# Kernel optimization log

Measured on AMD Instinct MI355X. Metric: run time of the kernel, lower is better.

The kernel has to match this reference:

```python
import jax, jax.numpy as jnp
import numpy as np

ARITY, LABEL_DIM, H_DIM, B = 2, 128, 512, 16384
ARG_DIM = LABEL_DIM + ARITY * H_DIM


def setup_inputs() -> dict:
    key = jax.random.key(0)
    ks = jax.random.split(key, 12)
    s_lin = 1.0 / np.sqrt(ARG_DIM)
    inp = {
        "label": jax.random.normal(ks[0], (B, LABEL_DIM), jnp.float32),
        "children_h": jax.random.normal(ks[1], (ARITY, B, H_DIM), jnp.float32),
        "children_c": jax.random.normal(ks[2], (ARITY, B, H_DIM), jnp.float32),
        # torch Linear params: W (h, arg_dim), b (h,)
        "W_i": jax.random.normal(ks[3], (H_DIM, ARG_DIM), jnp.float32) * s_lin,
        "b_i": jax.random.normal(ks[4], (H_DIM,), jnp.float32) * s_lin,
        "W_o": jax.random.normal(ks[5], (H_DIM, ARG_DIM), jnp.float32) * s_lin,
        "b_o": jax.random.normal(ks[6], (H_DIM,), jnp.float32) * s_lin,
        "W_u": jax.random.normal(ks[7], (H_DIM, ARG_DIM), jnp.float32) * s_lin,
        "b_u": jax.random.normal(ks[8], (H_DIM,), jnp.float32) * s_lin,
        # forget params (xavier-ish init)
        "W_fl": jax.random.normal(ks[9], (H_DIM, LABEL_DIM), jnp.float32) * np.sqrt(2.0 / (H_DIM + LABEL_DIM)),
        "W_fs": jax.random.normal(ks[10], (ARITY, ARITY, H_DIM, H_DIM), jnp.float32) * np.sqrt(1.0 / H_DIM),
        "forget_bias": jax.random.normal(ks[11], (H_DIM,), jnp.float32) * 0.1,
    }
    return inp


def reference(label, children_h, children_c, W_i, b_i, W_o, b_o, W_u, b_u, W_fl, W_fs, forget_bias):
    arity, b, h = children_h.shape
    # x = cat([label, h_0, ..., h_{arity-1}], dim=1)  -> (B, arg_dim)
    x = jnp.concatenate([label, children_h.transpose(1, 0, 2).reshape(b, arity * h)], axis=1)
    i_gate = jax.nn.sigmoid(x @ W_i.T + b_i)
    o_gate = jax.nn.sigmoid(x @ W_o.T + b_o)
    u = jnp.tanh(x @ W_u.T + b_u)
    # per-child forget weight: [W_fl | W_fs[k,0] | ... | W_fs[k,arity-1]]  -> (arity, h, arg_dim)
    Wf = jnp.concatenate(
        [jnp.broadcast_to(W_fl, (arity,) + W_fl.shape),
         W_fs.transpose(0, 2, 1, 3).reshape(arity, h, arity * h)],
        axis=2,
    )
    # bmm (no bias inside sigmoid; forget_bias enters separately below)
    f = jax.nn.sigmoid(jnp.einsum("khd,bd->kbh", Wf, x))
    cells_composed = (f * children_c).sum(axis=0)          # (B, h)
    cells_forget_bias = forget_bias * children_c.sum(axis=0)
    next_cell = i_gate * u + cells_composed + cells_forget_bias
    out = jnp.tanh(o_gate * next_cell)
    return (next_cell, out)
```

## Files before the change

### kernel.cpp

```cpp
#include <hip/hip_runtime.h>
#include <hip/hip_bf16.h>
#include <cstdint>
#include <cstddef>

#define BROWS   16384
#define LDIM    128
#define HDIM    512
#define KDIM    1152
#define NGATES  2560

#define XB_BYTES  ((size_t)BROWS * KDIM * 2)
#define WB_BYTES  ((size_t)NGATES * KDIM * 2)

using f32x4  = __attribute__((ext_vector_type(4))) float;
using bfrag  = __attribute__((ext_vector_type(8))) short;
using short4v = __attribute__((ext_vector_type(4))) short;

__device__ __forceinline__ short f2bf(float f) {
    union { float f; uint32_t u; } a; a.f = f;
    uint32_t u = a.u;
    uint32_t lsb = (u >> 16) & 1u;
    u += 0x7fffu + lsb;
    return (short)(u >> 16);
}
__device__ __forceinline__ float bf2f(short s) {
    union { uint32_t u; float f; } a;
    a.u = ((uint32_t)(uint16_t)s) << 16;
    return a.f;
}

__device__ __forceinline__ void load_lds16(const void* g, void* l) {
    __builtin_amdgcn_global_load_lds(
        (const __attribute__((address_space(1))) void*)g,
        (__attribute__((address_space(3))) void*)l, 16, 0, 0);
}

__global__ __launch_bounds__(256) void pack_x(const float* __restrict__ label,
                                              const float* __restrict__ chh,
                                              short* __restrict__ xb) {
    const int perRow = KDIM / 4;
    int tid = blockIdx.x * 256 + threadIdx.x;
    int b  = tid / perRow;
    int d4 = (tid - b * perRow) * 4;
    if (b >= BROWS) return;
    float4 v;
    if (d4 < LDIM) {
        v = *(const float4*)(label + (size_t)b * LDIM + d4);
    } else {
        int dd = d4 - LDIM;
        int k  = dd >> 9;
        int j  = dd & 511;
        v = *(const float4*)(chh + ((size_t)k * BROWS + b) * HDIM + j);
    }
    short4v s;
    s.x = f2bf(v.x); s.y = f2bf(v.y); s.z = f2bf(v.z); s.w = f2bf(v.w);
    *(short4v*)(xb + (size_t)b * KDIM + d4) = s;
}

__global__ __launch_bounds__(256) void pack_w(const float* __restrict__ Wi,
                                              const float* __restrict__ Wo,
                                              const float* __restrict__ Wu,
                                              const float* __restrict__ Wfl,
                                              const float* __restrict__ Wfs,
                                              short* __restrict__ Wb) {
    const int perRow = KDIM / 4;
    int tid = blockIdx.x * 256 + threadIdx.x;
    int n  = tid / perRow;
    int d4 = (tid - n * perRow) * 4;
    if (n >= NGATES) return;
    int g = n >> 9, h = n & 511;
    const float* src;
    if (g == 0)      src = Wi + (size_t)h * KDIM + d4;
    else if (g == 1) src = Wo + (size_t)h * KDIM + d4;
    else if (g == 2) src = Wu + (size_t)h * KDIM + d4;
    else {
        int k = g - 3;
        if (d4 < LDIM) {
            src = Wfl + (size_t)h * LDIM + d4;
        } else {
            int dd = d4 - LDIM;
            int j  = dd >> 9;
            int jj = dd & 511;
            src = Wfs + (((size_t)(k * 2 + j) * HDIM + h) * HDIM) + jj;
        }
    }
    float4 v = *(const float4*)src;
    short4v s;
    s.x = f2bf(v.x); s.y = f2bf(v.y); s.z = f2bf(v.z); s.w = f2bf(v.w);
    *(short4v*)(Wb + (size_t)n * KDIM + d4) = s;
}

__global__ __launch_bounds__(256) void gemm_bt(const short* __restrict__ A,
                                               const short* __restrict__ Bt,
                                               short* __restrict__ C) {
    __shared__ short As[128 * 32];
    __shared__ short Bs[128 * 32];

    const int t    = threadIdx.x;
    const int lane = t & 63;
    const int wave = t >> 6;
    const int wr   = wave >> 1;
    const int wc   = wave & 1;
    const int quad = lane >> 4;
    const int l16  = lane & 15;

    const int mBase = blockIdx.x * 128;
    const int nBase = blockIdx.y * 128;

    f32x4 acc[4][4] = {};

    const int s0 = t, s1 = t + 256;
    const int r0 = s0 >> 2, c0 = (s0 & 3) * 8;
    const int r1 = s1 >> 2, c1 = (s1 & 3) * 8;

    const short* Arow0 = A + (size_t)(mBase + r0) * KDIM + c0;
    const short* Arow1 = A + (size_t)(mBase + r1) * KDIM + c1;
    const short* Brow0 = Bt + (size_t)(nBase + r0) * KDIM + c0;
    const short* Brow1 = Bt + (size_t)(nBase + r1) * KDIM + c1;

    for (int k0 = 0; k0 < KDIM; k0 += 32) {
        load_lds16(Arow0 + k0, As + s0 * 8);
        load_lds16(Arow1 + k0, As + s1 * 8);
        load_lds16(Brow0 + k0, Bs + s0 * 8);
        load_lds16(Brow1 + k0, Bs + s1 * 8);
        __syncthreads();

        bfrag a[4], b[4];
#pragma unroll
        for (int i = 0; i < 4; ++i) {
            int rowA = wr * 64 + i * 16 + l16;
            a[i] = *(const bfrag*)(As + rowA * 32 + quad * 8);
            int rowB = wc * 64 + i * 16 + l16;
            b[i] = *(const bfrag*)(Bs + rowB * 32 + quad * 8);
        }
#pragma unroll
        for (int i = 0; i < 4; ++i)
#pragma unroll
            for (int j = 0; j < 4; ++j)
                acc[i][j] = __builtin_amdgcn_mfma_f32_16x16x32_bf16(a[i], b[j], acc[i][j], 0, 0, 0);
        __syncthreads();
    }

#pragma unroll
    for (int i = 0; i < 4; ++i) {
        int m0 = mBase + wr * 64 + i * 16 + quad * 4;
#pragma unroll
        for (int j = 0; j < 4; ++j) {
            int n = nBase + wc * 64 + j * 16 + l16;
#pragma unroll
            for (int r = 0; r < 4; ++r) {
                C[(size_t)(m0 + r) * NGATES + n] = f2bf(acc[i][j][r]);
            }
        }
    }
}

__device__ __forceinline__ float fast_sigmoid(float x) {
    return 1.0f / (1.0f + __expf(-x));
}
__device__ __forceinline__ float fast_tanh(float x) {
    float t = __expf(2.0f * x);
    return (t - 1.0f) / (t + 1.0f);
}

__global__ __launch_bounds__(256) void epilogue(const short* __restrict__ gates,
                                                const float* __restrict__ chc,
                                                const float* __restrict__ b_i,
                                                const float* __restrict__ b_o,
                                                const float* __restrict__ b_u,
                                                const float* __restrict__ fbias,
                                                float* __restrict__ out) {
    int idx = blockIdx.x * 256 + threadIdx.x;
    if (idx >= BROWS * HDIM) return;
    int b = idx >> 9;
    int h = idx & 511;
    const short* g = gates + (size_t)b * NGATES;
    float gi  = bf2f(g[h]);
    float go  = bf2f(g[HDIM + h]);
    float gu  = bf2f(g[2 * HDIM + h]);
    float gf0 = bf2f(g[3 * HDIM + h]);
    float gf1 = bf2f(g[4 * HDIM + h]);

    float ig = fast_sigmoid(gi + b_i[h]);
    float og = fast_sigmoid(go + b_o[h]);
    float uu = fast_tanh(gu + b_u[h]);
    float f0 = fast_sigmoid(gf0);
    float f1 = fast_sigmoid(gf1);

    float c0 = chc[idx];
    float c1 = chc[(size_t)BROWS * HDIM + idx];
    float fb = fbias[h];

    float ncell = ig * uu + f0 * c0 + f1 * c1 + fb * (c0 + c1);
    out[idx] = ncell;
    out[(size_t)BROWS * HDIM + idx] = fast_tanh(og * ncell);
}

extern "C" void kernel_launch(void* const* d_in, const int* in_sizes, int n_in,
                              void* d_out, int out_size, void* d_ws, size_t ws_size,
                              hipStream_t stream) {
    const float* label = (const float*)d_in[0];
    const float* chh   = (const float*)d_in[1];
    const float* chc   = (const float*)d_in[2];
    const float* W_i   = (const float*)d_in[3];
    const float* b_i   = (const float*)d_in[4];
    const float* W_o   = (const float*)d_in[5];
    const float* b_o   = (const float*)d_in[6];
    const float* W_u   = (const float*)d_in[7];
    const float* b_u   = (const float*)d_in[8];
    const float* W_fl  = (const float*)d_in[9];
    const float* W_fs  = (const float*)d_in[10];
    const float* fbias = (const float*)d_in[11];
    float* out = (float*)d_out;

    char* ws = (char*)d_ws;
    short* xb    = (short*)ws;
    short* Wb    = (short*)(ws + XB_BYTES);
    short* gates = (short*)(ws + XB_BYTES + WB_BYTES);

    pack_x<<<(BROWS * (KDIM / 4)) / 256, 256, 0, stream>>>(label, chh, xb);
    pack_w<<<(NGATES * (KDIM / 4)) / 256, 256, 0, stream>>>(W_i, W_o, W_u, W_fl, W_fs, Wb);
    dim3 ggrid(BROWS / 128, NGATES / 128);
    gemm_bt<<<ggrid, 256, 0, stream>>>(xb, Wb, gates);
    epilogue<<<(BROWS * HDIM) / 256, 256, 0, stream>>>(gates, chc, b_i, b_o, b_u, fbias, out);
}
```

Before: 334.5 us.

## Fuse gate GEMM with LSTM cell epilogue, computing five gates per tile sequentially

Replaces the separate GEMM and epilogue kernels with one kernel. Each block owns a 128-row by 128-hidden tile and runs five K-loops, one per gate, folding the activations into a register-resident next-cell accumulator before writing both outputs. This removes the bf16 gates buffer round trip and one launch, and avoids bf16 rounding of gate values. The cost is higher register pressure (ncell array plus accumulators, launch_bounds 256,2), a grid five times smaller in the N dimension, and uncoalesced column-strided chc loads and out stores in the epilogue.

New measurement: 448.0 us. 33.9% more time.

```diff
diff --git a/kernel.cpp b/kernel.cpp
--- a/kernel.cpp
+++ b/kernel.cpp
@@ -12,8 +12,8 @@
 #define XB_BYTES  ((size_t)BROWS * KDIM * 2)
 #define WB_BYTES  ((size_t)NGATES * KDIM * 2)
 
-using f32x4  = __attribute__((ext_vector_type(4))) float;
-using bfrag  = __attribute__((ext_vector_type(8))) short;
+using f32x4   = __attribute__((ext_vector_type(4))) float;
+using bfrag   = __attribute__((ext_vector_type(8))) short;
 using short4v = __attribute__((ext_vector_type(4))) short;
 
 __device__ __forceinline__ short f2bf(float f) {
@@ -23,16 +23,19 @@
     u += 0x7fffu + lsb;
     return (short)(u >> 16);
 }
-__device__ __forceinline__ float bf2f(short s) {
-    union { uint32_t u; float f; } a;
-    a.u = ((uint32_t)(uint16_t)s) << 16;
-    return a.f;
-}
 
 __device__ __forceinline__ void load_lds16(const void* g, void* l) {
     __builtin_amdgcn_global_load_lds(
         (const __attribute__((address_space(1))) void*)g,
         (__attribute__((address_space(3))) void*)l, 16, 0, 0);
+}
+
+__device__ __forceinline__ float fast_sigmoid(float x) {
+    return 1.0f / (1.0f + __expf(-x));
+}
+__device__ __forceinline__ float fast_tanh(float x) {
+    float t = __expf(2.0f * x);
+    return 1.0f - 2.0f / (t + 1.0f);
 }
 
 __global__ __launch_bounds__(256) void pack_x(const float* __restrict__ label,
@@ -90,9 +93,51 @@
     *(short4v*)(Wb + (size_t)n * KDIM + d4) = s;
 }
 
-__global__ __launch_bounds__(256) void gemm_bt(const short* __restrict__ A,
-                                               const short* __restrict__ Bt,
-                                               short* __restrict__ C) {
+__device__ __forceinline__ void run_gemm_pass(
+    const short* __restrict__ Arow0, const short* __restrict__ Arow1,
+    const short* __restrict__ Brow0, const short* __restrict__ Brow1,
+    short* As, short* Bs,
+    int s0, int s1, int wr, int wc, int quad, int l16,
+    f32x4 acc[4][4])
+{
+#pragma unroll
+    for (int i = 0; i < 4; ++i)
+#pragma unroll
+        for (int j = 0; j < 4; ++j)
+            acc[i][j] = (f32x4){0.f, 0.f, 0.f, 0.f};
+
+    for (int k0 = 0; k0 < KDIM; k0 += 32) {
+        load_lds16(Arow0 + k0, As + s0 * 8);
+        load_lds16(Arow1 + k0, As + s1 * 8);
+        load_lds16(Brow0 + k0, Bs + s0 * 8);
+        load_lds16(Brow1 + k0, Bs + s1 * 8);
+        __syncthreads();
+
+        bfrag a[4], b[4];
+#pragma unroll
+        for (int i = 0; i < 4; ++i) {
+            a[i] = *(const bfrag*)(As + (wr * 64 + i * 16 + l16) * 32 + quad * 8);
+            b[i] = *(const bfrag*)(Bs + (wc * 64 + i * 16 + l16) * 32 + quad * 8);
+        }
+#pragma unroll
+        for (int i = 0; i < 4; ++i)
+#pragma unroll
+            for (int j = 0; j < 4; ++j)
+                acc[i][j] = __builtin_amdgcn_mfma_f32_16x16x32_bf16(a[i], b[j], acc[i][j], 0, 0, 0);
+        __syncthreads();
+    }
+}
+
+__global__ __launch_bounds__(256, 2) void fused_cell(
+    const short* __restrict__ A,
+    const short* __restrict__ Wb,
+    const float* __restrict__ chc,
+    const float* __restrict__ b_i,
+    const float* __restrict__ b_o,
+    const float* __restrict__ b_u,
+    const float* __restrict__ fbias,
+    float* __restrict__ out)
+{
     __shared__ short As[128 * 32];
     __shared__ short Bs[128 * 32];
 
@@ -105,95 +150,106 @@
     const int l16  = lane & 15;
 
     const int mBase = blockIdx.x * 128;
-    const int nBase = blockIdx.y * 128;
-
-    f32x4 acc[4][4] = {};
+    const int hBase = blockIdx.y * 128;
 
     const int s0 = t, s1 = t + 256;
-    const int r0 = s0 >> 2, c0 = (s0 & 3) * 8;
-    const int r1 = s1 >> 2, c1 = (s1 & 3) * 8;
-
-    const short* Arow0 = A + (size_t)(mBase + r0) * KDIM + c0;
-    const short* Arow1 = A + (size_t)(mBase + r1) * KDIM + c1;
-    const short* Brow0 = Bt + (size_t)(nBase + r0) * KDIM + c0;
-    const short* Brow1 = Bt + (size_t)(nBase + r1) * KDIM + c1;
-
-    for (int k0 = 0; k0 < KDIM; k0 += 32) {
-        load_lds16(Arow0 + k0, As + s0 * 8);
-        load_lds16(Arow1 + k0, As + s1 * 8);
-        load_lds16(Brow0 + k0, Bs + s0 * 8);
-        load_lds16(Brow1 + k0, Bs + s1 * 8);
-        __syncthreads();
-
-        bfrag a[4], b[4];
-#pragma unroll
-        for (int i = 0; i < 4; ++i) {
-            int rowA = wr * 64 + i * 16 + l16;
-            a[i] = *(const bfrag*)(As + rowA * 32 + quad * 8);
-            int rowB = wc * 64 + i * 16 + l16;
-            b[i] = *(const bfrag*)(Bs + rowB * 32 + quad * 8);
-        }
+    const int r0 = s0 >> 2, c0s = (s0 & 3) * 8;
+    const int r1 = s1 >> 2, c1s = (s1 & 3) * 8;
+
+    const short* Arow0 = A + (size_t)(mBase + r0) * KDIM + c0s;
+    const short* Arow1 = A + (size_t)(mBase + r1) * KDIM + c1s;
+
+    float bi[4], bo[4], bu[4], fb[4];
+#pragma unroll
+    for (int j = 0; j < 4; ++j) {
+        int h = hBase + wc * 64 + j * 16 + l16;
+        bi[j] = b_i[h]; bo[j] = b_o[h]; bu[j] = b_u[h]; fb[j] = fbias[h];
+    }
+
+    f32x4 acc[4][4];
+    float ncell[4][4][4];
+
+    {
+        const short* Bt = Wb + (size_t)(0 * HDIM + hBase) * KDIM;
+        run_gemm_pass(Arow0, Arow1, Bt + (size_t)r0 * KDIM + c0s, Bt + (size_t)r1 * KDIM + c1s,
+                      As, Bs, s0, s1, wr, wc, quad, l16, acc);
 #pragma unroll
         for (int i = 0; i < 4; ++i)
 #pragma unroll
             for (int j = 0; j < 4; ++j)
-                acc[i][j] = __builtin_amdgcn_mfma_f32_16x16x32_bf16(a[i], b[j], acc[i][j], 0, 0, 0);
-        __syncthreads();
-    }
-
-#pragma unroll
-    for (int i = 0; i < 4; ++i) {
-        int m0 = mBase + wr * 64 + i * 16 + quad * 4;
-#pragma unroll
-        for (int j = 0; j < 4; ++j) {
-            int n = nBase + wc * 64 + j * 16 + l16;
-#pragma unroll
-            for (int r = 0; r < 4; ++r) {
-                C[(size_t)(m0 + r) * NGATES + n] = f2bf(acc[i][j][r]);
+#pragma unroll
+                for (int r = 0; r < 4; ++r)
+                    ncell[i][j][r] = fast_sigmoid(acc[i][j][r] + bi[j]);
+    }
+    {
+        const short* Bt = Wb + (size_t)(2 * HDIM + hBase) * KDIM;
+        run_gemm_pass(Arow0, Arow1, Bt + (size_t)r0 * KDIM + c0s, Bt + (size_t)r1 * KDIM + c1s,
+                      As, Bs, s0, s1, wr, wc, quad, l16, acc);
+#pragma unroll
+        for (int i = 0; i < 4; ++i)
+#pragma unroll
+            for (int j = 0; j < 4; ++j)
+#pragma unroll
+                for (int r = 0; r < 4; ++r)
+                    ncell[i][j][r] *= fast_tanh(acc[i][j][r] + bu[j]);
+    }
+    {
+        const short* Bt = Wb + (size_t)(3 * HDIM + hBase) * KDIM;
+        run_gemm_pass(Arow0, Arow1, Bt + (size_t)r0 * KDIM + c0s, Bt + (size_t)r1 * KDIM + c1s,
+                      As, Bs, s0, s1, wr, wc, quad, l16, acc);
+#pragma unroll
+        for (int i = 0; i < 4; ++i) {
+            int m0 = mBase + wr * 64 + i * 16 + quad * 4;
+#pragma unroll
+            for (int j = 0; j < 4; ++j) {
+                int h = hBase + wc * 64 + j * 16 + l16;
+#pragma unroll
+                for (int r = 0; r < 4; ++r) {
+                    float c0v = chc[(size_t)(m0 + r) * HDIM + h];
+                    ncell[i][j][r] += (fast_sigmoid(acc[i][j][r]) + fb[j]) * c0v;
+                }
             }
         }
     }
-}
-
-__device__ __forceinline__ float fast_sigmoid(float x) {
-    return 1.0f / (1.0f + __expf(-x));
-}
-__device__ __forceinline__ float fast_tanh(float x) {
-    float t = __expf(2.0f * x);
-    return (t - 1.0f) / (t + 1.0f);
-}
-
-__global__ __launch_bounds__(256) void epilogue(const short* __restrict__ gates,
-                                                const float* __restrict__ chc,
-                                                const float* __restrict__ b_i,
-                                                const float* __restrict__ b_o,
-                                                const float* __restrict__ b_u,
-                                                const float* __restrict__ fbias,
-                                                float* __restrict__ out) {
-    int idx = blockIdx.x * 256 + threadIdx.x;
-    if (idx >= BROWS * HDIM) return;
-    int b = idx >> 9;
-    int h = idx & 511;
-    const short* g = gates + (size_t)b * NGATES;
-    float gi  = bf2f(g[h]);
-    float go  = bf2f(g[HDIM + h]);
-    float gu  = bf2f(g[2 * HDIM + h]);
-    float gf0 = bf2f(g[3 * HDIM + h]);
-    float gf1 = bf2f(g[4 * HDIM + h]);
-
-    float ig = fast_sigmoid(gi + b_i[h]);
-    float og = fast_sigmoid(go + b_o[h]);
-    float uu = fast_tanh(gu + b_u[h]);
-    float f0 = fast_sigmoid(gf0);
-    float f1 = fast_sigmoid(gf1);
-
-    float c0 = chc[idx];
-    float c1 = chc[(size_t)BROWS * HDIM + idx];
-    float fb = fbias[h];
-
-    float ncell = ig * uu + f0 * c0 + f1 * c1 + fb * (c0 + c1);
-    out[idx] = ncell;
-    out[(size_t)BROWS * HDIM + idx] = fast_tanh(og * ncell);
+    {
+        const short* Bt = Wb + (size_t)(4 * HDIM + hBase) * KDIM;
+        run_gemm_pass(Arow0, Arow1, Bt + (size_t)r0 * KDIM + c0s, Bt + (size_t)r1 * KDIM + c1s,
+                      As, Bs, s0, s1, wr, wc, quad, l16, acc);
+#pragma unroll
+        for (int i = 0; i < 4; ++i) {
+            int m0 = mBase + wr * 64 + i * 16 + quad * 4;
+#pragma unroll
+            for (int j = 0; j < 4; ++j) {
+                int h = hBase + wc * 64 + j * 16 + l16;
+#pragma unroll
+                for (int r = 0; r < 4; ++r) {
+                    float c1v = chc[(size_t)BROWS * HDIM + (size_t)(m0 + r) * HDIM + h];
+                    float nc = ncell[i][j][r] + (fast_sigmoid(acc[i][j][r]) + fb[j]) * c1v;
+                    ncell[i][j][r] = nc;
+                    out[(size_t)(m0 + r) * HDIM + h] = nc;
+                }
+            }
+        }
+    }
+    {
+        const short* Bt = Wb + (size_t)(1 * HDIM + hBase) * KDIM;
+        run_gemm_pass(Arow0, Arow1, Bt + (size_t)r0 * KDIM + c0s, Bt + (size_t)r1 * KDIM + c1s,
+                      As, Bs, s0, s1, wr, wc, quad, l16, acc);
+#pragma unroll
+        for (int i = 0; i < 4; ++i) {
+            int m0 = mBase + wr * 64 + i * 16 + quad * 4;
+#pragma unroll
+            for (int j = 0; j < 4; ++j) {
+                int h = hBase + wc * 64 + j * 16 + l16;
+#pragma unroll
+                for (int r = 0; r < 4; ++r) {
+                    float og = fast_sigmoid(acc[i][j][r] + bo[j]);
+                    out[(size_t)BROWS * HDIM + (size_t)(m0 + r) * HDIM + h] =
+                        fast_tanh(og * ncell[i][j][r]);
+                }
+            }
+        }
+    }
 }
 
 extern "C" void kernel_launch(void* const* d_in, const int* in_sizes, int n_in,
@@ -214,13 +270,12 @@
     float* out = (float*)d_out;
 
     char* ws = (char*)d_ws;
-    short* xb    = (short*)ws;
-    short* Wb    = (short*)(ws + XB_BYTES);
-    short* gates = (short*)(ws + XB_BYTES + WB_BYTES);
+    short* xb = (short*)ws;
+    short* Wb = (short*)(ws + XB_BYTES);
 
     pack_x<<<(BROWS * (KDIM / 4)) / 256, 256, 0, stream>>>(label, chh, xb);
     pack_w<<<(NGATES * (KDIM / 4)) / 256, 256, 0, stream>>>(W_i, W_o, W_u, W_fl, W_fs, Wb);
-    dim3 ggrid(BROWS / 128, NGATES / 128);
-    gemm_bt<<<ggrid, 256, 0, stream>>>(xb, Wb, gates);
-    epilogue<<<(BROWS * HDIM) / 256, 256, 0, stream>>>(gates, chc, b_i, b_o, b_u, fbias, out);
-}
+
+    dim3 ggrid(BROWS / 128, HDIM / 128);
+    fused_cell<<<ggrid, 256, 0, stream>>>(xb, Wb, chc, b_i, b_o, b_u, fbias, out);
+}
```
